# Performance work log

Measured on AMD Instinct MI355X. Metric: run time of the kernel, lower is better.

## Reference

```python
import jax, jax.numpy as jnp
import numpy as np

EMBED = 1024
HEADS = 16
HEAD_DIM = EMBED // HEADS
FF = 4096
B, T = 2, 2048


def setup_inputs() -> dict:
    key = jax.random.key(0)
    ks = jax.random.split(key, 12)
    s = lambda k, shape, fan: jax.random.normal(k, shape, jnp.float32) * (1.0 / np.sqrt(fan))
    return {
        "x": jax.random.normal(ks[0], (B, T, EMBED), jnp.float32),
        "qkv_w": s(ks[1], (EMBED, 3 * EMBED), EMBED),
        "qkv_b": jnp.zeros((3 * EMBED,), jnp.float32),
        "out_w": s(ks[2], (EMBED, EMBED), EMBED),
        "out_b": jnp.zeros((EMBED,), jnp.float32),
        "ff_w1": s(ks[3], (EMBED, FF), EMBED),
        "ff_b1": jnp.zeros((FF,), jnp.float32),
        "ff_w2": s(ks[4], (FF, EMBED), FF),
        "ff_b2": jnp.zeros((EMBED,), jnp.float32),
        "ln1_g": jnp.ones((EMBED,), jnp.float32),
        "ln1_b": jnp.zeros((EMBED,), jnp.float32),
        "ln2_g": jnp.ones((EMBED,), jnp.float32),
        "ln2_b": jnp.zeros((EMBED,), jnp.float32),
    }


def _layer_norm(x, g, b, eps=1e-5):
    mu = jnp.mean(x, axis=-1, keepdims=True)
    var = jnp.var(x, axis=-1, keepdims=True)
    return (x - mu) * jax.lax.rsqrt(var + eps) * g + b


def _attention(x, qkv_w, qkv_b, out_w, out_b):
    Bv, Tv, C = x.shape
    qkv = x @ qkv_w + qkv_b                      # [B,T,3C]
    qkv = qkv.reshape(Bv, Tv, 3, HEADS, HEAD_DIM)
    q, k, v = qkv[:, :, 0], qkv[:, :, 1], qkv[:, :, 2]  # [B,T,H,D]
    scale = 1.0 / np.sqrt(HEAD_DIM)
    scores = jnp.einsum("bqhd,bkhd->bhqk", q, k) * scale  # [B,H,T,T]
    attn = jax.nn.softmax(scores, axis=-1)
    out = jnp.einsum("bhqk,bkhd->bqhd", attn, v).reshape(Bv, Tv, C)
    return out @ out_w + out_b


def _ffn(x, w1, b1, w2, b2):
    h = jax.nn.gelu(x @ w1 + b1, approximate=False)
    return h @ w2 + b2


def reference(x, qkv_w, qkv_b, out_w, out_b, ff_w1, ff_b1, ff_w2, ff_b2,
              ln1_g, ln1_b, ln2_g, ln2_b):
    x = x + _attention(_layer_norm(x, ln1_g, ln1_b), qkv_w, qkv_b, out_w, out_b)
    x = x + _ffn(_layer_norm(x, ln2_g, ln2_b), ff_w1, ff_b1, ff_w2, ff_b2)
    return x
```

## Files before the change

kernel.cpp:

```cpp
#include <hip/hip_runtime.h>

#define E     1024
#define HEADS 16
#define HD    64
#define FFD   4096
#define TT    2048
#define MMDIM 4096
#define NKV   1024
#define PO    (32 * 2048 * 64)

typedef __bf16 bf16x8 __attribute__((ext_vector_type(8)));
typedef float f32x4 __attribute__((ext_vector_type(4)));
typedef float f32x16 __attribute__((ext_vector_type(16)));
typedef unsigned short u16;
typedef unsigned u32;
typedef u16 ushort8 __attribute__((ext_vector_type(8)));
typedef u16 us4 __attribute__((ext_vector_type(4)));
typedef u32 u32x4 __attribute__((ext_vector_type(4)));

__device__ __forceinline__ u16 f2bf(float f) {
  unsigned u = __float_as_uint(f);
  u = (u + 0x7fffu + ((u >> 16) & 1u)) >> 16;
  return (u16)u;
}
__device__ __forceinline__ float bf2f(u16 u) {
  return __uint_as_float(((unsigned)u) << 16);
}
__device__ __forceinline__ u32 cvtpk(float a, float b) {
  u32 r;
  asm("v_cvt_pk_bf16_f32 %0, %1, %2" : "=v"(r) : "v"(a), "v"(b));
  return r;
}

__device__ __forceinline__ void gload_lds16(const void* g, void* l) {
  __builtin_amdgcn_global_load_lds((__attribute__((address_space(1))) void*)g,
                                   (__attribute__((address_space(3))) void*)l,
                                   16, 0, 0);
}

__global__ void __launch_bounds__(256) ln_kernel(const float* __restrict__ x,
                                                 const float* __restrict__ g,
                                                 const float* __restrict__ b,
                                                 u16* __restrict__ out) {
  int row = blockIdx.x;
  int t = threadIdx.x;
  const float4 v = reinterpret_cast<const float4*>(x + (size_t)row * E)[t];
  float s = v.x + v.y + v.z + v.w;
  float s2 = v.x * v.x + v.y * v.y + v.z * v.z + v.w * v.w;
#pragma unroll
  for (int m = 1; m < 64; m <<= 1) {
    s += __shfl_xor(s, m);
    s2 += __shfl_xor(s2, m);
  }
  __shared__ float red[8];
  int wave = t >> 6, lane = t & 63;
  if (lane == 0) { red[wave] = s; red[wave + 4] = s2; }
  __syncthreads();
  s = red[0] + red[1] + red[2] + red[3];
  s2 = red[4] + red[5] + red[6] + red[7];
  float mean = s * (1.f / E);
  float var = s2 * (1.f / E) - mean * mean;
  float inv = rsqrtf(var + 1e-5f);
  const float4 gv = reinterpret_cast<const float4*>(g)[t];
  const float4 bv = reinterpret_cast<const float4*>(b)[t];
  us4 pk;
  pk.x = f2bf((v.x - mean) * inv * gv.x + bv.x);
  pk.y = f2bf((v.y - mean) * inv * gv.y + bv.y);
  pk.z = f2bf((v.z - mean) * inv * gv.z + bv.z);
  pk.w = f2bf((v.w - mean) * inv * gv.w + bv.w);
  *(us4*)(out + (size_t)row * E + t * 4) = pk;
}

__global__ void __launch_bounds__(256) transpose_bf16(const float* __restrict__ in,
                                                      u16* __restrict__ out,
                                                      int K, int N) {
  __shared__ float tile[32][33];
  int k0 = blockIdx.y * 32, n0 = blockIdx.x * 32;
  int tx = threadIdx.x, ty = threadIdx.y;
#pragma unroll
  for (int i = ty; i < 32; i += 8)
    tile[i][tx] = in[(size_t)(k0 + i) * N + n0 + tx];
  __syncthreads();
#pragma unroll
  for (int i = ty; i < 32; i += 8)
    out[(size_t)(n0 + i) * K + k0 + tx] = f2bf(tile[tx][i]);
}

template <int MODE>
__global__ void __launch_bounds__(256) gemm2p(const u16* __restrict__ Aa,
                                              const u16* __restrict__ Bt,
                                              const float* __restrict__ bias,
                                              const float* __restrict__ resid,
                                              u16* __restrict__ ob0,
                                              u16* __restrict__ ob1,
                                              u16* __restrict__ ob2,
                                              float* __restrict__ of,
                                              int N, int K, int lda, int ldb) {
  __shared__ __align__(16) u16 As[2][128 * 64];
  __shared__ __align__(16) u16 Bs[2][128 * 64];
  const int n0 = blockIdx.x * 128, m0 = blockIdx.y * 128;
  const int tid = threadIdx.x, lane = tid & 63;
  const int wave = tid >> 6, wr = wave >> 1, wc = wave & 1;
  const int l15 = lane & 15, hi4 = lane >> 4, l7 = lane & 7;
  const size_t koff = (size_t)blockIdx.z * K;
  const int nt = K >> 6;

  f32x4 acc[4][4];
#pragma unroll
  for (int i = 0; i < 4; i++)
#pragma unroll
    for (int j = 0; j < 4; j++) acc[i][j] = (f32x4){0.f, 0.f, 0.f, 0.f};

  const u16* ApR[4];
  const u16* BpR[4];
#pragma unroll
  for (int r = 0; r < 4; r++) {
    int c = tid + r * 256;
    int row = c >> 3;
    int col = ((c & 7) ^ (row & 7)) * 8;
    ApR[r] = Aa + (size_t)(m0 + row) * lda + koff + col;
    BpR[r] = Bt + (size_t)(n0 + row) * ldb + koff + col;
  }

  const int xk0 = (hi4 << 4) ^ (l7 << 4);
  const int xk1 = (64 + (hi4 << 4)) ^ (l7 << 4);

#define STAGE2P(T, BUF)                                                        \
  do {                                                                         \
    int k0_ = (T) << 6;                                                        \
    _Pragma("unroll") for (int r_ = 0; r_ < 4; r_++) {                         \
      int c_ = tid + r_ * 256;                                                 \
      gload_lds16(ApR[r_] + k0_, &As[BUF][c_ * 8]);                            \
      gload_lds16(BpR[r_] + k0_, &Bs[BUF][c_ * 8]);                            \
    }                                                                          \
  } while (0)

  STAGE2P(0, 0);
  asm volatile("s_waitcnt vmcnt(0)" ::: "memory");
  __builtin_amdgcn_s_barrier();
  __builtin_amdgcn_sched_barrier(0);

  for (int t = 0; t < nt; ++t) {
    const int cur = t & 1;
    if (t + 1 < nt) {
      if (cur == 0) STAGE2P(t + 1, 1);
      else          STAGE2P(t + 1, 0);
    }
    const char* ab = (const char*)&As[0][0] + cur * 16384;
    const char* bb = (const char*)&Bs[0][0] + cur * 16384;
    bf16x8 a0[4], a1[4], b0[4], b1[4];
#pragma unroll
    for (int i = 0; i < 4; i++) {
      int rowb = (wr * 64 + i * 16 + l15) * 128;
      a0[i] = *(const bf16x8*)(ab + rowb + xk0);
      a1[i] = *(const bf16x8*)(ab + rowb + xk1);
    }
#pragma unroll
    for (int j = 0; j < 4; j++) {
      int rowb = (wc * 64 + j * 16 + l15) * 128;
      b0[j] = *(const bf16x8*)(bb + rowb + xk0);
      b1[j] = *(const bf16x8*)(bb + rowb + xk1);
    }
    asm volatile("s_waitcnt lgkmcnt(0)" ::: "memory");
    __builtin_amdgcn_sched_barrier(0);
    __builtin_amdgcn_s_setprio(1);
#pragma unroll
    for (int i = 0; i < 4; i++)
#pragma unroll
      for (int j = 0; j < 4; j++) {
        acc[i][j] = __builtin_amdgcn_mfma_f32_16x16x32_bf16(a0[i], b0[j], acc[i][j], 0, 0, 0);
        acc[i][j] = __builtin_amdgcn_mfma_f32_16x16x32_bf16(a1[i], b1[j], acc[i][j], 0, 0, 0);
      }
    __builtin_amdgcn_s_setprio(0);
    asm volatile("s_waitcnt vmcnt(0)" ::: "memory");
    __builtin_amdgcn_s_barrier();
    __builtin_amdgcn_sched_barrier(0);
  }
#undef STAGE2P

#pragma unroll
  for (int i = 0; i < 4; i++) {
#pragma unroll
    for (int j = 0; j < 4; j++) {
      int mb = m0 + wr * 64 + i * 16 + (hi4 << 2);
      int n = n0 + wc * 64 + j * 16 + l15;
      float bv = (MODE == 3) ? 0.f : bias[n];
      float v4[4];
#pragma unroll
      for (int r = 0; r < 4; r++) v4[r] = acc[i][j][r] + bv;
      if (MODE == 0) {
        int b_ = mb >> 11;
        int t = mb & 2047;
        int s = n >> 10;
        int hd = n & 1023;
        int h_ = hd >> 6;
        int d = hd & 63;
        size_t bh = (size_t)b_ * HEADS + h_;
        if (s == 0) {
#pragma unroll
          for (int r = 0; r < 4; r++)
            ob0[(bh * TT + (t + r)) * HD + d] = f2bf(v4[r] * 0.125f);
        } else if (s == 1) {
#pragma unroll
          for (int r = 0; r < 4; r++)
            ob1[(bh * TT + (t + r)) * HD + d] = f2bf(v4[r]);
        } else {
          us4 pk;
#pragma unroll
          for (int r = 0; r < 4; r++) pk[r] = f2bf(v4[r]);
          *(us4*)&ob2[(bh * HD + d) * TT + t] = pk;
        }
      } else if (MODE == 1) {
#pragma unroll
        for (int r = 0; r < 4; r++) {
          size_t idx = (size_t)(mb + r) * E + n;
          of[idx] = v4[r] + resid[idx];
        }
      } else if (MODE == 2) {
#pragma unroll
        for (int r = 0; r < 4; r++)
          ob0[(size_t)(mb + r) * FFD + n] =
              f2bf(0.5f * v4[r] * (1.f + erff(v4[r] * 0.70710678118f)));
      } else {
        if (blockIdx.z == 0) {
          float bz = bias[n];
#pragma unroll
          for (int r = 0; r < 4; r++) {
            size_t idx = (size_t)(mb + r) * E + n;
            of[idx] = v4[r] + bz + resid[idx];
          }
        } else {
#pragma unroll
          for (int r = 0; r < 4; r++)
            ob0[(size_t)(mb + r) * N + n] = f2bf(v4[r]);
        }
      }
    }
  }
}

__global__ void __launch_bounds__(256) ff2_reduce(const u16* __restrict__ p1,
                                                  float* __restrict__ out) {
  size_t i = ((size_t)blockIdx.x * 256 + threadIdx.x) * 4;
  us4 a = *(const us4*)(p1 + i);
  float4 o = *(const float4*)(out + i);
  o.x += bf2f(a.x);
  o.y += bf2f(a.y);
  o.z += bf2f(a.z);
  o.w += bf2f(a.w);
  *(float4*)(out + i) = o;
}

__global__ void __launch_bounds__(512, 4) attn_kernel(const u16* __restrict__ Qb,
                                                      const u16* __restrict__ Kb,
                                                      const u16* __restrict__ Vt,
                                                      u16* __restrict__ op,
                                                      float2* __restrict__ ml) {
  __shared__ __align__(16) u16 Ks[2][64 * 64];
  __shared__ __align__(16) u16 Vs[2][64 * 64];
  const int bid = blockIdx.x;
  const int bh = bid & 31;
  const int qblk = (bid >> 5) & 7;
  const int part = bid >> 8;
  const int pstart = part * NKV;
  const int tid = threadIdx.x;
  const int w = tid >> 6, lane = tid & 63;
  const int lq = lane & 31, hi = lane >> 5;
  const int q0 = qblk * 256 + w * 32;

  const u16* Qp = Qb + ((size_t)bh * TT + q0 + lq) * HD + hi * 8;
  bf16x8 qf[4];
#pragma unroll
  for (int c = 0; c < 4; c++) qf[c] = *(const bf16x8*)(Qp + c * 16);

  const int srow = tid >> 3, schk = tid & 7;
  const u16* Kg = Kb + ((size_t)bh * TT + pstart + srow) * HD + ((schk ^ (srow & 7)) * 8);
  const u16* Vg = Vt + ((size_t)bh * HD + srow) * TT + pstart + ((schk ^ (srow & 7)) * 8);
  u16* kdst = &Ks[0][0] + tid * 8;
  u16* vdst = &Vs[0][0] + tid * 8;

  int ofs[8];
#pragma unroll
  for (int c = 0; c < 8; c++) ofs[c] = (c ^ (lq & 7)) << 4;

  f32x16 o0, o1;
#pragma unroll
  for (int r = 0; r < 16; r++) { o0[r] = 0.f; o1[r] = 0.f; }
  float m_run = -1e30f, l_run = 0.f;

#define STAGEKV(T, BUF)                                                        \
  do {                                                                         \
    gload_lds16(Kg + (size_t)(T) * 64 * HD, kdst + (BUF) * 4096);              \
    gload_lds16(Vg + (T) * 64, vdst + (BUF) * 4096);                           \
  } while (0)

  STAGEKV(0, 0);
  asm volatile("s_waitcnt vmcnt(0)" ::: "memory");
  __builtin_amdgcn_s_barrier();
  __builtin_amdgcn_sched_barrier(0);

  const int NT = NKV / 64;
  for (int t = 0; t < NT; ++t) {
    const int buf = t & 1;
    if (t + 1 < NT) STAGEKV(t + 1, buf ^ 1);
    const char* kT = (const char*)&Ks[buf][0];
    const char* vT = (const char*)&Vs[buf][0];
#pragma unroll
    for (int ss = 0; ss < 2; ++ss) {
      const char* kR = kT + (ss * 32 + lq) * 128;
      bf16x8 kf[4];
#pragma unroll
      for (int c = 0; c < 4; c++) kf[c] = *(const bf16x8*)(kR + ofs[c * 2 + hi]);
      const char* vR0 = vT + lq * 128;
      const char* vR1 = vT + (32 + lq) * 128;
      bf16x8 v00 = *(const bf16x8*)(vR0 + ofs[ss * 4 + 0 + hi]);
      bf16x8 v01 = *(const bf16x8*)(vR0 + ofs[ss * 4 + 2 + hi]);
      bf16x8 v10 = *(const bf16x8*)(vR1 + ofs[ss * 4 + 0 + hi]);
      bf16x8 v11 = *(const bf16x8*)(vR1 + ofs[ss * 4 + 2 + hi]);
      asm volatile("s_waitcnt lgkmcnt(0)" ::: "memory");
      __builtin_amdgcn_sched_barrier(0);

      f32x16 s;
#pragma unroll
      for (int r = 0; r < 16; r++) s[r] = 0.f;
      __builtin_amdgcn_s_setprio(1);
#pragma unroll
      for (int c = 0; c < 4; c++)
        s = __builtin_amdgcn_mfma_f32_32x32x16_bf16(kf[c], qf[c], s, 0, 0, 0);
      __builtin_amdgcn_s_setprio(0);

      float mx = s[0];
#pragma unroll
      for (int r = 1; r < 16; r++) mx = fmaxf(mx, s[r]);
      mx = fmaxf(mx, __shfl_xor(mx, 32));

      if (__any(mx > m_run + 8.f)) {
        float mn = fmaxf(m_run, mx);
        float al = __expf(m_run - mn);
#pragma unroll
        for (int r = 0; r < 16; r++) { o0[r] *= al; o1[r] *= al; }
        l_run *= al;
        m_run = mn;
      }

      float p[16], ps = 0.f;
#pragma unroll
      for (int r = 0; r < 16; r++) {
        p[r] = __expf(s[r] - m_run);
        ps += p[r];
      }
      l_run += ps + __shfl_xor(ps, 32);

      u32 wv[8];
#pragma unroll
      for (int c = 0; c < 2; c++) {
        u32 qA = cvtpk(p[c * 8 + 0], p[c * 8 + 1]);
        u32 qB = cvtpk(p[c * 8 + 2], p[c * 8 + 3]);
        u32 qC = cvtpk(p[c * 8 + 4], p[c * 8 + 5]);
        u32 qD = cvtpk(p[c * 8 + 6], p[c * 8 + 7]);
        u32 As_ = __shfl_xor(qA, 32), Bs_ = __shfl_xor(qB, 32);
        u32 Cs_ = __shfl_xor(qC, 32), Ds_ = __shfl_xor(qD, 32);
        wv[c * 4 + 0] = hi ? Cs_ : qA;
        wv[c * 4 + 1] = hi ? Ds_ : qB;
        wv[c * 4 + 2] = hi ? qC : As_;
        wv[c * 4 + 3] = hi ? qD : Bs_;
      }
      u32x4 t0 = {wv[0], wv[1], wv[2], wv[3]};
      u32x4 t1 = {wv[4], wv[5], wv[6], wv[7]};
      bf16x8 pf0 = __builtin_bit_cast(bf16x8, t0);
      bf16x8 pf1 = __builtin_bit_cast(bf16x8, t1);

      __builtin_amdgcn_s_setprio(1);
      o0 = __builtin_amdgcn_mfma_f32_32x32x16_bf16(v00, pf0, o0, 0, 0, 0);
      o0 = __builtin_amdgcn_mfma_f32_32x32x16_bf16(v01, pf1, o0, 0, 0, 0);
      o1 = __builtin_amdgcn_mfma_f32_32x32x16_bf16(v10, pf0, o1, 0, 0, 0);
      o1 = __builtin_amdgcn_mfma_f32_32x32x16_bf16(v11, pf1, o1, 0, 0, 0);
      __builtin_amdgcn_s_setprio(0);
    }
    asm volatile("s_waitcnt vmcnt(0)" ::: "memory");
    __builtin_amdgcn_s_barrier();
    __builtin_amdgcn_sched_barrier(0);
  }
#undef STAGEKV

  float rl = 1.f / l_run;
  u16* opP = op + (size_t)part * PO + ((size_t)bh * TT + q0 + lq) * HD;
#pragma unroll
  for (int r = 0; r < 16; r++) {
    int d = (r & 3) + ((r >> 2) << 3) + (hi << 2);
    opP[d] = f2bf(o0[r] * rl);
    opP[32 + d] = f2bf(o1[r] * rl);
  }
  if (hi == 0) {
    float2 v;
    v.x = m_run;
    v.y = l_run;
    ml[(size_t)part * (32 * TT) + bh * TT + q0 + lq] = v;
  }
}

__global__ void __launch_bounds__(256) attn_merge(const u16* __restrict__ op,
                                                  const float2* __restrict__ ml,
                                                  u16* __restrict__ O) {
  int idx = blockIdx.x * 256 + threadIdx.x;
  int bh = idx >> 14;
  int q = (idx >> 3) & 2047;
  int d0 = (idx & 7) * 8;
  int mli = bh * TT + q;
  float2 ab0 = ml[mli];
  float2 ab1 = ml[32 * TT + mli];
  float ms = fmaxf(ab0.x, ab1.x);
  float w0 = ab0.y * __expf(ab0.x - ms);
  float w1 = ab1.y * __expf(ab1.x - ms);
  float inv = 1.f / (w0 + w1);
  w0 *= inv;
  w1 *= inv;
  size_t base = ((size_t)bh * TT + q) * HD + d0;
  ushort8 a = *(const ushort8*)(op + base);
  ushort8 b = *(const ushort8*)(op + PO + base);
  ushort8 o;
#pragma unroll
  for (int k = 0; k < 8; k++) o[k] = f2bf(w0 * bf2f(a[k]) + w1 * bf2f(b[k]));
  size_t obase = ((size_t)(bh >> 4) * TT + q) * E + (bh & 15) * HD + d0;
  *(ushort8*)(O + obase) = o;
}

extern "C" void kernel_launch(void* const* d_in, const int* in_sizes, int n_in,
                              void* d_out, int out_size, void* d_ws, size_t ws_size,
                              hipStream_t stream) {
  (void)in_sizes; (void)n_in; (void)out_size; (void)ws_size;
  const float* x = (const float*)d_in[0];
  const float* qkv_w = (const float*)d_in[1];
  const float* qkv_b = (const float*)d_in[2];
  const float* out_w = (const float*)d_in[3];
  const float* out_b = (const float*)d_in[4];
  const float* ff_w1 = (const float*)d_in[5];
  const float* ff_b1 = (const float*)d_in[6];
  const float* ff_w2 = (const float*)d_in[7];
  const float* ff_b2 = (const float*)d_in[8];
  const float* ln1_g = (const float*)d_in[9];
  const float* ln1_b = (const float*)d_in[10];
  const float* ln2_g = (const float*)d_in[11];
  const float* ln2_b = (const float*)d_in[12];

  char* ws = (char*)d_ws;
  u16* outwt = (u16*)(ws + 0);
  u16* ffw1t = (u16*)(ws + 2097152);
  u16* ffw2t = (u16*)(ws + 10485760);
  u16* qkvwt = (u16*)(ws + 18874368);
  u16* ln_out = (u16*)(ws + 25165824);
  float* x1 = (float*)(ws + 33554432);
  u16* qb = (u16*)(ws + 50331648);
  u16* kb = (u16*)(ws + 58720256);
  u16* vt = (u16*)(ws + 67108864);
  u16* attn_o = (u16*)(ws + 75497472);
  u16* opbuf = (u16*)(ws + 18874368);
  float2* mlbuf = (float2*)(ws + 35651584);
  u16* hbuf = (u16*)(ws + 50331648);
  u16* pbuf = (u16*)(ws + 0);

  dim3 tb(32, 8);
  transpose_bf16<<<dim3(3072 / 32, 1024 / 32), tb, 0, stream>>>(qkv_w, qkvwt, 1024, 3072);
  transpose_bf16<<<dim3(1024 / 32, 1024 / 32), tb, 0, stream>>>(out_w, outwt, 1024, 1024);
  transpose_bf16<<<dim3(4096 / 32, 1024 / 32), tb, 0, stream>>>(ff_w1, ffw1t, 1024, 4096);
  transpose_bf16<<<dim3(1024 / 32, 4096 / 32), tb, 0, stream>>>(ff_w2, ffw2t, 4096, 1024);

  ln_kernel<<<MMDIM, 256, 0, stream>>>(x, ln1_g, ln1_b, ln_out);
  gemm2p<0><<<dim3(3072 / 128, MMDIM / 128), 256, 0, stream>>>(
      ln_out, qkvwt, qkv_b, nullptr, qb, kb, vt, nullptr, 3072, 1024, 1024, 1024);
  attn_kernel<<<dim3(2 * 8 * 32), 512, 0, stream>>>(qb, kb, vt, opbuf, mlbuf);
  attn_merge<<<dim3(32 * TT * 8 / 256), 256, 0, stream>>>(opbuf, mlbuf, attn_o);
  gemm2p<1><<<dim3(1024 / 128, MMDIM / 128), 256, 0, stream>>>(
      attn_o, outwt, out_b, x, nullptr, nullptr, nullptr, x1, 1024, 1024, 1024, 1024);
  ln_kernel<<<MMDIM, 256, 0, stream>>>(x1, ln2_g, ln2_b, ln_out);
  gemm2p<2><<<dim3(4096 / 128, MMDIM / 128), 256, 0, stream>>>(
      ln_out, ffw1t, ff_b1, nullptr, hbuf, nullptr, nullptr, nullptr, 4096, 1024, 1024, 1024);
  gemm2p<3><<<dim3(1024 / 128, MMDIM / 128, 2), 256, 0, stream>>>(
      hbuf, ffw2t, ff_b2, x1, pbuf, nullptr, nullptr, (float*)d_out, 1024, 2048, 4096, 4096);
  ff2_reduce<<<(size_t)MMDIM * E / 1024, 256, 0, stream>>>(pbuf, (float*)d_out);
}
```

Measured before the change: 285.2 us.

## Add 256x256-tile GEMM kernel and split-K for out-proj and FF2

Adds a 512-thread GEMM with 256x256 output tiles and 128KB dynamic LDS double buffering, used for the QKV, FF1 and FF2 matmuls to raise operand reuse per block. The output projection becomes a 2-way split-K with a separate bf16 partial reduce, and FF2 moves from 2-way to 4-way split-K with a combined reduction over three partial buffers placed in reused workspace regions. Larger tiles cut the block count (e.g. 192 blocks for QKV), which may leave CUs idle on a 256-CU part. The bf16 partials add rounding error and extra memory traffic.

```diff
diff --git a/kernel.cpp b/kernel.cpp
--- a/kernel.cpp
+++ b/kernel.cpp
@@ -87,13 +87,182 @@
 }
 
 template <int MODE>
+__global__ void __launch_bounds__(512, 2)
+gemm256(const u16* __restrict__ Aa, const u16* __restrict__ Bt,
+        const float* __restrict__ bias, const float* __restrict__ resid,
+        u16* __restrict__ ob0, u16* __restrict__ ob1, u16* __restrict__ ob2,
+        float* __restrict__ of, u16* __restrict__ p1, u16* __restrict__ p2,
+        u16* __restrict__ p3a, u16* __restrict__ p3b,
+        int N, int K, int lda, int ldb) {
+  extern __shared__ char lds[];
+  const int n0 = blockIdx.x * 256, m0 = blockIdx.y * 256;
+  const int tid = threadIdx.x, lane = tid & 63;
+  const int w = tid >> 6, wr = w >> 2, wc = w & 3;
+  const int l15 = lane & 15, hi4 = lane >> 4;
+  const size_t koff = (size_t)blockIdx.z * K;
+  const int nt = K >> 6;
+
+  f32x4 acc[8][4];
+#pragma unroll
+  for (int i = 0; i < 8; i++)
+#pragma unroll
+    for (int j = 0; j < 4; j++) acc[i][j] = (f32x4){0.f, 0.f, 0.f, 0.f};
+
+  const u16* ApR[4];
+  const u16* BpR[4];
+  int cch[4];
+#pragma unroll
+  for (int r = 0; r < 4; r++) {
+    int c = tid + r * 512;
+    int row = c >> 3;
+    int col = ((c & 7) ^ (row & 7)) * 8;
+    cch[r] = c;
+    ApR[r] = Aa + (size_t)(m0 + row) * lda + koff + col;
+    BpR[r] = Bt + (size_t)(n0 + row) * ldb + koff + col;
+  }
+
+  const int rx = (l15 & 7) << 4;
+  const int ka0 = (hi4 << 4) ^ rx;
+  const int ka1 = (64 + (hi4 << 4)) ^ rx;
+
+#define STG256(T, BUF)                                                         \
+  do {                                                                         \
+    int k0_ = (T) << 6;                                                        \
+    char* base_ = lds + (BUF) * 65536;                                         \
+    _Pragma("unroll") for (int r_ = 0; r_ < 4; r_++) {                         \
+      gload_lds16(ApR[r_] + k0_, base_ + cch[r_] * 16);                        \
+      gload_lds16(BpR[r_] + k0_, base_ + 32768 + cch[r_] * 16);                \
+    }                                                                          \
+  } while (0)
+
+  STG256(0, 0);
+  asm volatile("s_waitcnt vmcnt(0)" ::: "memory");
+  __builtin_amdgcn_s_barrier();
+  __builtin_amdgcn_sched_barrier(0);
+
+  for (int t = 0; t < nt; ++t) {
+    const int cur = t & 1;
+    if (t + 1 < nt) {
+      if (cur == 0) STG256(t + 1, 1);
+      else          STG256(t + 1, 0);
+    }
+    const char* ab = lds + cur * 65536;
+    const char* bb = ab + 32768;
+    bf16x8 bfr[4][2], af[4][2];
+#pragma unroll
+    for (int nj = 0; nj < 4; nj++) {
+      int rowb = (wc * 64 + nj * 16 + l15) * 128;
+      bfr[nj][0] = *(const bf16x8*)(bb + rowb + ka0);
+      bfr[nj][1] = *(const bf16x8*)(bb + rowb + ka1);
+    }
+#pragma unroll
+    for (int mi = 0; mi < 4; mi++) {
+      int rowa = (wr * 128 + mi * 16 + l15) * 128;
+      af[mi][0] = *(const bf16x8*)(ab + rowa + ka0);
+      af[mi][1] = *(const bf16x8*)(ab + rowa + ka1);
+    }
+    asm volatile("s_waitcnt lgkmcnt(0)" ::: "memory");
+    __builtin_amdgcn_sched_barrier(0);
+    __builtin_amdgcn_s_setprio(1);
+#pragma unroll
+    for (int mi = 0; mi < 4; mi++)
+#pragma unroll
+      for (int nj = 0; nj < 4; nj++) {
+        acc[mi][nj] = __builtin_amdgcn_mfma_f32_16x16x32_bf16(af[mi][0], bfr[nj][0], acc[mi][nj], 0, 0, 0);
+        acc[mi][nj] = __builtin_amdgcn_mfma_f32_16x16x32_bf16(af[mi][1], bfr[nj][1], acc[mi][nj], 0, 0, 0);
+      }
+    __builtin_amdgcn_s_setprio(0);
+#pragma unroll
+    for (int mi = 0; mi < 4; mi++) {
+      int rowa = (wr * 128 + (mi + 4) * 16 + l15) * 128;
+      af[mi][0] = *(const bf16x8*)(ab + rowa + ka0);
+      af[mi][1] = *(const bf16x8*)(ab + rowa + ka1);
+    }
+    asm volatile("s_waitcnt lgkmcnt(0)" ::: "memory");
+    __builtin_amdgcn_sched_barrier(0);
+    __builtin_amdgcn_s_setprio(1);
+#pragma unroll
+    for (int mi = 0; mi < 4; mi++)
+#pragma unroll
+      for (int nj = 0; nj < 4; nj++) {
+        acc[mi + 4][nj] = __builtin_amdgcn_mfma_f32_16x16x32_bf16(af[mi][0], bfr[nj][0], acc[mi + 4][nj], 0, 0, 0);
+        acc[mi + 4][nj] = __builtin_amdgcn_mfma_f32_16x16x32_bf16(af[mi][1], bfr[nj][1], acc[mi + 4][nj], 0, 0, 0);
+      }
+    __builtin_amdgcn_s_setprio(0);
+    asm volatile("s_waitcnt vmcnt(0)" ::: "memory");
+    __builtin_amdgcn_s_barrier();
+    __builtin_amdgcn_sched_barrier(0);
+  }
+#undef STG256
+
+#pragma unroll
+  for (int mi = 0; mi < 8; mi++) {
+#pragma unroll
+    for (int nj = 0; nj < 4; nj++) {
+      int mb = m0 + wr * 128 + mi * 16 + (hi4 << 2);
+      int n = n0 + wc * 64 + nj * 16 + l15;
+      float bv = (MODE == 3) ? 0.f : bias[n];
+      float v4[4];
+#pragma unroll
+      for (int r = 0; r < 4; r++) v4[r] = acc[mi][nj][r] + bv;
+      if (MODE == 0) {
+        int b_ = mb >> 11;
+        int t = mb & 2047;
+        int s = n >> 10;
+        int hd = n & 1023;
+        int h_ = hd >> 6;
+        int d = hd & 63;
+        size_t bh = (size_t)b_ * HEADS + h_;
+        if (s == 0) {
+#pragma unroll
+          for (int r = 0; r < 4; r++)
+            ob0[(bh * TT + (t + r)) * HD + d] = f2bf(v4[r] * 0.125f);
+        } else if (s == 1) {
+#pragma unroll
+          for (int r = 0; r < 4; r++)
+            ob1[(bh * TT + (t + r)) * HD + d] = f2bf(v4[r]);
+        } else {
+          us4 pk;
+#pragma unroll
+          for (int r = 0; r < 4; r++) pk[r] = f2bf(v4[r]);
+          *(us4*)&ob2[(bh * HD + d) * TT + t] = pk;
+        }
+      } else if (MODE == 2) {
+#pragma unroll
+        for (int r = 0; r < 4; r++)
+          ob0[(size_t)(mb + r) * FFD + n] =
+              f2bf(0.5f * v4[r] * (1.f + erff(v4[r] * 0.70710678118f)));
+      } else {
+        int z = blockIdx.z;
+        if (z == 0) {
+          float bz = bias[n];
+#pragma unroll
+          for (int r = 0; r < 4; r++) {
+            size_t idx = (size_t)(mb + r) * E + n;
+            of[idx] = v4[r] + bz + resid[idx];
+          }
+        } else {
+          u16* pz;
+          int mrow = mb;
+          if (z == 1) pz = p1;
+          else if (z == 2) pz = p2;
+          else if (mb < 3072) pz = p3a;
+          else { pz = p3b; mrow = mb - 3072; }
+#pragma unroll
+          for (int r = 0; r < 4; r++)
+            pz[(size_t)(mrow + r) * N + n] = f2bf(v4[r]);
+        }
+      }
+    }
+  }
+}
+
+template <int MODE>
 __global__ void __launch_bounds__(256) gemm2p(const u16* __restrict__ Aa,
                                               const u16* __restrict__ Bt,
                                               const float* __restrict__ bias,
                                               const float* __restrict__ resid,
                                               u16* __restrict__ ob0,
-                                              u16* __restrict__ ob1,
-                                              u16* __restrict__ ob2,
                                               float* __restrict__ of,
                                               int N, int K, int lda, int ldb) {
   __shared__ __align__(16) u16 As[2][128 * 64];
@@ -184,70 +353,52 @@
     for (int j = 0; j < 4; j++) {
       int mb = m0 + wr * 64 + i * 16 + (hi4 << 2);
       int n = n0 + wc * 64 + j * 16 + l15;
-      float bv = (MODE == 3) ? 0.f : bias[n];
-      float v4[4];
-#pragma unroll
-      for (int r = 0; r < 4; r++) v4[r] = acc[i][j][r] + bv;
-      if (MODE == 0) {
-        int b_ = mb >> 11;
-        int t = mb & 2047;
-        int s = n >> 10;
-        int hd = n & 1023;
-        int h_ = hd >> 6;
-        int d = hd & 63;
-        size_t bh = (size_t)b_ * HEADS + h_;
-        if (s == 0) {
-#pragma unroll
-          for (int r = 0; r < 4; r++)
-            ob0[(bh * TT + (t + r)) * HD + d] = f2bf(v4[r] * 0.125f);
-        } else if (s == 1) {
-#pragma unroll
-          for (int r = 0; r < 4; r++)
-            ob1[(bh * TT + (t + r)) * HD + d] = f2bf(v4[r]);
-        } else {
-          us4 pk;
-#pragma unroll
-          for (int r = 0; r < 4; r++) pk[r] = f2bf(v4[r]);
-          *(us4*)&ob2[(bh * HD + d) * TT + t] = pk;
-        }
-      } else if (MODE == 1) {
-#pragma unroll
-        for (int r = 0; r < 4; r++) {
-          size_t idx = (size_t)(mb + r) * E + n;
-          of[idx] = v4[r] + resid[idx];
-        }
-      } else if (MODE == 2) {
-#pragma unroll
-        for (int r = 0; r < 4; r++)
-          ob0[(size_t)(mb + r) * FFD + n] =
-              f2bf(0.5f * v4[r] * (1.f + erff(v4[r] * 0.70710678118f)));
-      } else {
+      if (MODE == 5) {
         if (blockIdx.z == 0) {
           float bz = bias[n];
 #pragma unroll
           for (int r = 0; r < 4; r++) {
             size_t idx = (size_t)(mb + r) * E + n;
-            of[idx] = v4[r] + bz + resid[idx];
+            of[idx] = acc[i][j][r] + bz + resid[idx];
           }
         } else {
 #pragma unroll
           for (int r = 0; r < 4; r++)
-            ob0[(size_t)(mb + r) * N + n] = f2bf(v4[r]);
+            ob0[(size_t)(mb + r) * N + n] = f2bf(acc[i][j][r]);
         }
       }
     }
   }
 }
 
-__global__ void __launch_bounds__(256) ff2_reduce(const u16* __restrict__ p1,
-                                                  float* __restrict__ out) {
+__global__ void __launch_bounds__(256) proj_reduce(const u16* __restrict__ p,
+                                                   float* __restrict__ out) {
   size_t i = ((size_t)blockIdx.x * 256 + threadIdx.x) * 4;
-  us4 a = *(const us4*)(p1 + i);
+  us4 a = *(const us4*)(p + i);
   float4 o = *(const float4*)(out + i);
   o.x += bf2f(a.x);
   o.y += bf2f(a.y);
   o.z += bf2f(a.z);
   o.w += bf2f(a.w);
+  *(float4*)(out + i) = o;
+}
+
+__global__ void __launch_bounds__(256) ff2_reduce4(const u16* __restrict__ p1,
+                                                   const u16* __restrict__ p2,
+                                                   const u16* __restrict__ p3a,
+                                                   const u16* __restrict__ p3b,
+                                                   float* __restrict__ out) {
+  size_t i = ((size_t)blockIdx.x * 256 + threadIdx.x) * 4;
+  int row = (int)(i >> 10);
+  const u16* p3 = (row < 3072) ? (p3a + i) : (p3b + (i - (size_t)3072 * 1024));
+  us4 a = *(const us4*)(p1 + i);
+  us4 b = *(const us4*)(p2 + i);
+  us4 c = *(const us4*)p3;
+  float4 o = *(const float4*)(out + i);
+  o.x += bf2f(a.x) + bf2f(b.x) + bf2f(c.x);
+  o.y += bf2f(a.y) + bf2f(b.y) + bf2f(c.y);
+  o.z += bf2f(a.z) + bf2f(b.z) + bf2f(c.z);
+  o.w += bf2f(a.w) + bf2f(b.w) + bf2f(c.w);
   *(float4*)(out + i) = o;
 }
 
@@ -457,7 +608,18 @@
   u16* opbuf = (u16*)(ws + 18874368);
   float2* mlbuf = (float2*)(ws + 35651584);
   u16* hbuf = (u16*)(ws + 50331648);
-  u16* pbuf = (u16*)(ws + 0);
+  u16* pproj = (u16*)(ws + 25165824);
+  u16* pf1 = (u16*)(ws + 0);
+  u16* pf2 = (u16*)(ws + 18874368);
+  u16* pf3a = (u16*)(ws + 27262976);
+  u16* pf3b = (u16*)(ws + 8388608);
+
+  hipFuncSetAttribute((const void*)gemm256<0>,
+                      hipFuncAttributeMaxDynamicSharedMemorySize, 131072);
+  hipFuncSetAttribute((const void*)gemm256<2>,
+                      hipFuncAttributeMaxDynamicSharedMemorySize, 131072);
+  hipFuncSetAttribute((const void*)gemm256<3>,
+                      hipFuncAttributeMaxDynamicSharedMemorySize, 131072);
 
   dim3 tb(32, 8);
   transpose_bf16<<<dim3(3072 / 32, 1024 / 32), tb, 0, stream>>>(qkv_w, qkvwt, 1024, 3072);
@@ -466,16 +628,21 @@
   transpose_bf16<<<dim3(1024 / 32, 4096 / 32), tb, 0, stream>>>(ff_w2, ffw2t, 4096, 1024);
 
   ln_kernel<<<MMDIM, 256, 0, stream>>>(x, ln1_g, ln1_b, ln_out);
-  gemm2p<0><<<dim3(3072 / 128, MMDIM / 128), 256, 0, stream>>>(
-      ln_out, qkvwt, qkv_b, nullptr, qb, kb, vt, nullptr, 3072, 1024, 1024, 1024);
+  gemm256<0><<<dim3(12, 16), 512, 131072, stream>>>(
+      ln_out, qkvwt, qkv_b, nullptr, qb, kb, vt, nullptr,
+      nullptr, nullptr, nullptr, nullptr, 3072, 1024, 1024, 1024);
   attn_kernel<<<dim3(2 * 8 * 32), 512, 0, stream>>>(qb, kb, vt, opbuf, mlbuf);
   attn_merge<<<dim3(32 * TT * 8 / 256), 256, 0, stream>>>(opbuf, mlbuf, attn_o);
-  gemm2p<1><<<dim3(1024 / 128, MMDIM / 128), 256, 0, stream>>>(
-      attn_o, outwt, out_b, x, nullptr, nullptr, nullptr, x1, 1024, 1024, 1024, 1024);
+  gemm2p<5><<<dim3(1024 / 128, MMDIM / 128, 2), 256, 0, stream>>>(
+      attn_o, outwt, out_b, x, pproj, x1, 1024, 512, 1024, 1024);
+  proj_reduce<<<(size_t)MMDIM * E / 1024, 256, 0, stream>>>(pproj, x1);
   ln_kernel<<<MMDIM, 256, 0, stream>>>(x1, ln2_g, ln2_b, ln_out);
-  gemm2p<2><<<dim3(4096 / 128, MMDIM / 128), 256, 0, stream>>>(
-      ln_out, ffw1t, ff_b1, nullptr, hbuf, nullptr, nullptr, nullptr, 4096, 1024, 1024, 1024);
-  gemm2p<3><<<dim3(1024 / 128, MMDIM / 128, 2), 256, 0, stream>>>(
-      hbuf, ffw2t, ff_b2, x1, pbuf, nullptr, nullptr, (float*)d_out, 1024, 2048, 4096, 4096);
-  ff2_reduce<<<(size_t)MMDIM * E / 1024, 256, 0, stream>>>(pbuf, (float*)d_out);
-}
+  gemm256<2><<<dim3(16, 16), 512, 131072, stream>>>(
+      ln_out, ffw1t, ff_b1, nullptr, hbuf, nullptr, nullptr, nullptr,
+      nullptr, nullptr, nullptr, nullptr, 4096, 1024, 1024, 1024);
+  gemm256<3><<<dim3(4, 16, 4), 512, 131072, stream>>>(
+      hbuf, ffw2t, ff_b2, x1, nullptr, nullptr, nullptr, (float*)d_out,
+      pf1, pf2, pf3a, pf3b, 1024, 1024, 4096, 4096);
+  ff2_reduce4<<<(size_t)MMDIM * E / 1024, 256, 0, stream>>>(pf1, pf2, pf3a, pf3b,
+                                                            (float*)d_out);
+}
```

Result: slower. 354.1 us (+24.2%).

## Switch GEMM to 4-buffer K=32 pipeline with two stages in flight

Applied to the files above, without the earlier changes.

The GEMM k-tile drops from 64 to 32 and now uses four LDS buffers, so two future stages stay in flight while the current one is computed. The wait changes from a full vmcnt(0) drain to vmcnt(4), which leaves the next stage's loads outstanding. The XOR swizzle on LDS addresses is removed, so the 64-byte-stride fragment reads may hit more bank conflicts. Each iteration now does half the MFMA work per barrier, which doubles barrier count per unit of compute.

```diff
diff --git a/kernel.cpp b/kernel.cpp
--- a/kernel.cpp
+++ b/kernel.cpp
@@ -87,7 +87,7 @@
 }
 
 template <int MODE>
-__global__ void __launch_bounds__(256) gemm2p(const u16* __restrict__ Aa,
+__global__ void __launch_bounds__(256) gemm4b(const u16* __restrict__ Aa,
                                               const u16* __restrict__ Bt,
                                               const float* __restrict__ bias,
                                               const float* __restrict__ resid,
@@ -96,14 +96,14 @@
                                               u16* __restrict__ ob2,
                                               float* __restrict__ of,
                                               int N, int K, int lda, int ldb) {
-  __shared__ __align__(16) u16 As[2][128 * 64];
-  __shared__ __align__(16) u16 Bs[2][128 * 64];
+  __shared__ __align__(16) u16 As[4][128 * 32];
+  __shared__ __align__(16) u16 Bs[4][128 * 32];
   const int n0 = blockIdx.x * 128, m0 = blockIdx.y * 128;
   const int tid = threadIdx.x, lane = tid & 63;
   const int wave = tid >> 6, wr = wave >> 1, wc = wave & 1;
-  const int l15 = lane & 15, hi4 = lane >> 4, l7 = lane & 7;
+  const int l15 = lane & 15, hi4 = lane >> 4;
   const size_t koff = (size_t)blockIdx.z * K;
-  const int nt = K >> 6;
+  const int nt = K >> 5;
 
   f32x4 acc[4][4];
 #pragma unroll
@@ -111,72 +111,59 @@
 #pragma unroll
     for (int j = 0; j < 4; j++) acc[i][j] = (f32x4){0.f, 0.f, 0.f, 0.f};
 
-  const u16* ApR[4];
-  const u16* BpR[4];
-#pragma unroll
-  for (int r = 0; r < 4; r++) {
+  const u16* ApR[2];
+  const u16* BpR[2];
+  int cst[2];
+#pragma unroll
+  for (int r = 0; r < 2; r++) {
     int c = tid + r * 256;
-    int row = c >> 3;
-    int col = ((c & 7) ^ (row & 7)) * 8;
-    ApR[r] = Aa + (size_t)(m0 + row) * lda + koff + col;
-    BpR[r] = Bt + (size_t)(n0 + row) * ldb + koff + col;
-  }
-
-  const int xk0 = (hi4 << 4) ^ (l7 << 4);
-  const int xk1 = (64 + (hi4 << 4)) ^ (l7 << 4);
-
-#define STAGE2P(T, BUF)                                                        \
+    int row = c >> 2, ch = c & 3;
+    cst[r] = c;
+    ApR[r] = Aa + (size_t)(m0 + row) * lda + koff + ch * 8;
+    BpR[r] = Bt + (size_t)(n0 + row) * ldb + koff + ch * 8;
+  }
+
+#define STAGE4B(T)                                                             \
   do {                                                                         \
-    int k0_ = (T) << 6;                                                        \
-    _Pragma("unroll") for (int r_ = 0; r_ < 4; r_++) {                         \
-      int c_ = tid + r_ * 256;                                                 \
-      gload_lds16(ApR[r_] + k0_, &As[BUF][c_ * 8]);                            \
-      gload_lds16(BpR[r_] + k0_, &Bs[BUF][c_ * 8]);                            \
+    int buf_ = (T) & 3;                                                        \
+    int k0_ = (T) << 5;                                                        \
+    _Pragma("unroll") for (int r_ = 0; r_ < 2; r_++) {                         \
+      gload_lds16(ApR[r_] + k0_, (char*)&As[buf_][0] + cst[r_] * 16);          \
+      gload_lds16(BpR[r_] + k0_, (char*)&Bs[buf_][0] + cst[r_] * 16);          \
     }                                                                          \
   } while (0)
 
-  STAGE2P(0, 0);
-  asm volatile("s_waitcnt vmcnt(0)" ::: "memory");
+  STAGE4B(0);
+  STAGE4B(1);
+  asm volatile("s_waitcnt vmcnt(4)" ::: "memory");
   __builtin_amdgcn_s_barrier();
   __builtin_amdgcn_sched_barrier(0);
 
   for (int t = 0; t < nt; ++t) {
-    const int cur = t & 1;
-    if (t + 1 < nt) {
-      if (cur == 0) STAGE2P(t + 1, 1);
-      else          STAGE2P(t + 1, 0);
-    }
-    const char* ab = (const char*)&As[0][0] + cur * 16384;
-    const char* bb = (const char*)&Bs[0][0] + cur * 16384;
-    bf16x8 a0[4], a1[4], b0[4], b1[4];
-#pragma unroll
-    for (int i = 0; i < 4; i++) {
-      int rowb = (wr * 64 + i * 16 + l15) * 128;
-      a0[i] = *(const bf16x8*)(ab + rowb + xk0);
-      a1[i] = *(const bf16x8*)(ab + rowb + xk1);
-    }
-#pragma unroll
-    for (int j = 0; j < 4; j++) {
-      int rowb = (wc * 64 + j * 16 + l15) * 128;
-      b0[j] = *(const bf16x8*)(bb + rowb + xk0);
-      b1[j] = *(const bf16x8*)(bb + rowb + xk1);
-    }
+    if (t + 2 < nt) STAGE4B(t + 2);
+    const char* ab = (const char*)&As[t & 3][0];
+    const char* bb = (const char*)&Bs[t & 3][0];
+    bf16x8 a[4], b[4];
+#pragma unroll
+    for (int i = 0; i < 4; i++)
+      a[i] = *(const bf16x8*)(ab + (wr * 64 + i * 16 + l15) * 64 + hi4 * 16);
+#pragma unroll
+    for (int j = 0; j < 4; j++)
+      b[j] = *(const bf16x8*)(bb + (wc * 64 + j * 16 + l15) * 64 + hi4 * 16);
     asm volatile("s_waitcnt lgkmcnt(0)" ::: "memory");
     __builtin_amdgcn_sched_barrier(0);
     __builtin_amdgcn_s_setprio(1);
 #pragma unroll
     for (int i = 0; i < 4; i++)
 #pragma unroll
-      for (int j = 0; j < 4; j++) {
-        acc[i][j] = __builtin_amdgcn_mfma_f32_16x16x32_bf16(a0[i], b0[j], acc[i][j], 0, 0, 0);
-        acc[i][j] = __builtin_amdgcn_mfma_f32_16x16x32_bf16(a1[i], b1[j], acc[i][j], 0, 0, 0);
-      }
+      for (int j = 0; j < 4; j++)
+        acc[i][j] = __builtin_amdgcn_mfma_f32_16x16x32_bf16(a[i], b[j], acc[i][j], 0, 0, 0);
     __builtin_amdgcn_s_setprio(0);
-    asm volatile("s_waitcnt vmcnt(0)" ::: "memory");
+    asm volatile("s_waitcnt vmcnt(4)" ::: "memory");
     __builtin_amdgcn_s_barrier();
     __builtin_amdgcn_sched_barrier(0);
   }
-#undef STAGE2P
+#undef STAGE4B
 
 #pragma unroll
   for (int i = 0; i < 4; i++) {
@@ -466,16 +453,16 @@
   transpose_bf16<<<dim3(1024 / 32, 4096 / 32), tb, 0, stream>>>(ff_w2, ffw2t, 4096, 1024);
 
   ln_kernel<<<MMDIM, 256, 0, stream>>>(x, ln1_g, ln1_b, ln_out);
-  gemm2p<0><<<dim3(3072 / 128, MMDIM / 128), 256, 0, stream>>>(
+  gemm4b<0><<<dim3(3072 / 128, MMDIM / 128), 256, 0, stream>>>(
       ln_out, qkvwt, qkv_b, nullptr, qb, kb, vt, nullptr, 3072, 1024, 1024, 1024);
   attn_kernel<<<dim3(2 * 8 * 32), 512, 0, stream>>>(qb, kb, vt, opbuf, mlbuf);
   attn_merge<<<dim3(32 * TT * 8 / 256), 256, 0, stream>>>(opbuf, mlbuf, attn_o);
-  gemm2p<1><<<dim3(1024 / 128, MMDIM / 128), 256, 0, stream>>>(
+  gemm4b<1><<<dim3(1024 / 128, MMDIM / 128), 256, 0, stream>>>(
       attn_o, outwt, out_b, x, nullptr, nullptr, nullptr, x1, 1024, 1024, 1024, 1024);
   ln_kernel<<<MMDIM, 256, 0, stream>>>(x1, ln2_g, ln2_b, ln_out);
-  gemm2p<2><<<dim3(4096 / 128, MMDIM / 128), 256, 0, stream>>>(
+  gemm4b<2><<<dim3(4096 / 128, MMDIM / 128), 256, 0, stream>>>(
       ln_out, ffw1t, ff_b1, nullptr, hbuf, nullptr, nullptr, nullptr, 4096, 1024, 1024, 1024);
-  gemm2p<3><<<dim3(1024 / 128, MMDIM / 128, 2), 256, 0, stream>>>(
+  gemm4b<3><<<dim3(1024 / 128, MMDIM / 128, 2), 256, 0, stream>>>(
       hbuf, ffw2t, ff_b2, x1, pbuf, nullptr, nullptr, (float*)d_out, 1024, 2048, 4096, 4096);
   ff2_reduce<<<(size_t)MMDIM * E / 1024, 256, 0, stream>>>(pbuf, (float*)d_out);
 }
```

Measured after the change: 298.1 us. 1.05x slower.
